# Performance work log

Measured on AMD Instinct MI355X. Metric: run time of the kernel, lower is better.

## Reference

```python
import jax, jax.numpy as jnp
import numpy as np

# dims (see shape_source)
B, L_IN, L_C, H, D, BLOCK = 4, 512, 512, 32, 128, 16
CTX = L_IN + L_C                      # context length per sequence
BLOCKS_PER_SEQ = CTX // BLOCK         # 64
NUM_BLOCKS = B * BLOCKS_PER_SEQ       # 256
T = B * L_IN                          # total new tokens


def setup_inputs() -> dict:
    key = jax.random.key(0)
    ks = jax.random.split(key, 5)
    Q = jax.random.normal(ks[0], (T, H * D), jnp.float32)
    K = jax.random.normal(ks[1], (T, H * D), jnp.float32)
    V = jax.random.normal(ks[2], (T, H * D), jnp.float32)
    Kcache = jax.random.normal(ks[3], (NUM_BLOCKS, BLOCK, H, D), jnp.float32)
    Vcache = jax.random.normal(ks[4], (NUM_BLOCKS, BLOCK, H, D), jnp.float32)
    # rotary tables for the new tokens: seq b token i sits at position L_C+i
    inv = 1.0 / (10000.0 ** (np.arange(0, D, 2, dtype=np.float32) / D))
    pos = np.tile(np.arange(L_C, L_C + L_IN, dtype=np.float32), B)   # [T]
    ang = pos[:, None] * inv[None, :]                                # [T, D/2]
    cos = jnp.asarray(np.concatenate([np.cos(ang), np.cos(ang)], -1))
    sin = jnp.asarray(np.concatenate([np.sin(ang), np.sin(ang)], -1))
    mask = jnp.zeros((L_IN, CTX), jnp.float32)  # additive mask (causal added inside)
    input_length = jnp.full((B,), L_IN, jnp.int32)
    cache_length = jnp.full((B,), L_C, jnp.int32)
    block_tables = jnp.arange(NUM_BLOCKS, dtype=jnp.int32).reshape(B, BLOCKS_PER_SEQ)
    # slot of new token i of seq b = flat cache index inside seq b's blocks
    slot_np = (np.arange(B)[:, None] * CTX + (L_C + np.arange(L_IN))[None, :]).reshape(-1)
    slots = jnp.asarray(slot_np, jnp.int32)
    return dict(Q=Q, K=K, V=V, Kcache=Kcache, Vcache=Vcache, cos=cos, sin=sin,
                mask=mask, input_length=input_length, cache_length=cache_length,
                slots=slots, block_tables=block_tables, max_s=CTX)


def _rot_half(x):
    h = x.shape[-1] // 2
    return jnp.concatenate([-x[..., h:], x[..., :h]], -1)


def reference(Q, K, V, Kcache, Vcache, cos, sin, mask,
              input_length, cache_length, slots, block_tables, max_s):
    scale = 1.0 / np.sqrt(D).astype(np.float32)
    q = Q.reshape(T, H, D)
    k = K.reshape(T, H, D)
    v = V.reshape(T, H, D)
    # inline RoPE on Q and new K (cos/sin broadcast over heads, as in the op)
    c = cos[:, None, :]
    s = sin[:, None, :]
    q = q * c + _rot_half(q) * s
    k = k * c + _rot_half(k) * s
    # write new K/V into the paged cache at `slots` (mode 3 behaviour)
    kc = Kcache.reshape(NUM_BLOCKS * BLOCK, H, D).at[slots].set(k)
    vc = Vcache.reshape(NUM_BLOCKS * BLOCK, H, D).at[slots].set(v)
    # gather per-sequence context via block tables -> [B, CTX, H, D]
    offs = jnp.arange(BLOCK, dtype=block_tables.dtype)
    flat = (block_tables[:, :, None] * BLOCK + offs[None, None, :]).reshape(B, -1)
    keys = kc[flat]
    vals = vc[flat]
    qb = q.reshape(B, L_IN, H, D)
    scores = jnp.einsum('bqhd,bkhd->bhqk', qb, keys) * scale + mask[None, None]
    # causal + length masking: query i at global pos cache_length+i
    qpos = cache_length[:, None] + jnp.arange(L_IN, dtype=jnp.int32)   # [B, L_IN]
    kpos = jnp.arange(CTX, dtype=jnp.int32)
    valid = (kpos[None, None, :] <= qpos[:, :, None]) & \
            (kpos[None, None, :] < (cache_length + input_length)[:, None, None])
    scores = jnp.where(valid[:, None], scores, jnp.float32(-1e30))
    attn = jax.nn.softmax(scores, axis=-1)
    out = jnp.einsum('bhqk,bkhd->bqhd', attn, vals)
    return out.reshape(T, H * D)
```

## Files before the change

### kernel.cpp

```cpp
#include <hip/hip_runtime.h>
#include <stdint.h>

#define BB   4
#define LIN  512
#define LCC  512
#define CTXL 1024
#define HH   32
#define DDIM 128
#define HD   4096
#define TT   2048
#define SCALE 0.08838834764831845f

typedef __attribute__((ext_vector_type(8))) short bf16x8;
typedef __attribute__((ext_vector_type(4))) float f32x4;
typedef __attribute__((ext_vector_type(4))) unsigned short us4;

__device__ __forceinline__ unsigned short f2bf(float f) {
  unsigned u = __float_as_uint(f);
  u += 0x7fffu + ((u >> 16) & 1u);
  return (unsigned short)(u >> 16);
}

__device__ __forceinline__ void async16(const void* g, void* l) {
  __builtin_amdgcn_global_load_lds(
      (const __attribute__((address_space(1))) void*)g,
      (__attribute__((address_space(3))) void*)l, 16, 0, 0);
}

__global__ __launch_bounds__(256) void prep_rope(
    const float* __restrict__ Q, const float* __restrict__ K,
    const float* __restrict__ cosT, const float* __restrict__ sinT,
    unsigned short* __restrict__ Qr, unsigned short* __restrict__ Kc) {
  int idx = blockIdx.x * 256 + threadIdx.x;
  int dp = idx & 63;
  int h  = (idx >> 6) & 31;
  int t  = idx >> 11;
  int b  = t >> 9;
  int i  = t & 511;
  int srcBase = t * HD + h * DDIM;
  float c = cosT[t * DDIM + dp];
  float s = sinT[t * DDIM + dp];
  float q0 = Q[srcBase + dp], q1 = Q[srcBase + dp + 64];
  float k0 = K[srcBase + dp], k1 = K[srcBase + dp + 64];
  int bh = b * HH + h;
  unsigned short* qd = Qr + ((size_t)bh * LIN + i) * DDIM;
  qd[dp]      = f2bf((q0 * c - q1 * s) * SCALE);
  qd[dp + 64] = f2bf((q1 * c + q0 * s) * SCALE);
  unsigned short* kd = Kc + ((size_t)bh * CTXL + LCC + i) * DDIM;
  kd[dp]      = f2bf(k0 * c - k1 * s);
  kd[dp + 64] = f2bf(k1 * c + k0 * s);
}

__global__ __launch_bounds__(256) void prep_kcache(
    const float* __restrict__ Kcache, const int* __restrict__ btab,
    unsigned short* __restrict__ Kc) {
  int idx = blockIdx.x * 256 + threadIdx.x;
  int d4  = idx & 31;
  int h   = (idx >> 5) & 31;
  int pos = (idx >> 10) & 511;
  int b   = idx >> 19;
  int blk = btab[b * 64 + (pos >> 4)];
  size_t src = (((size_t)blk * 16 + (pos & 15)) * HH + h) * DDIM + d4 * 4;
  float4 k4 = *(const float4*)(Kcache + src);
  size_t dst = (((size_t)(b * HH + h)) * CTXL + pos) * DDIM + d4 * 4;
  us4 kp;
  kp[0] = f2bf(k4.x); kp[1] = f2bf(k4.y); kp[2] = f2bf(k4.z); kp[3] = f2bf(k4.w);
  *(us4*)(Kc + dst) = kp;
}

__global__ __launch_bounds__(256) void prep_vt(
    const float* __restrict__ V, const float* __restrict__ Vcache,
    const int* __restrict__ btab, unsigned short* __restrict__ Vt) {
  __shared__ unsigned short tile[64][128];
  int bh = blockIdx.x;
  int kt = blockIdx.y;
  int b = bh >> 5, h = bh & 31;
  int t = threadIdx.x;
  int kv0 = kt * 64;
  int col4  = (t & 31) * 4;
  int rbase = t >> 5;
#pragma unroll
  for (int r8 = 0; r8 < 8; ++r8) {
    int row = r8 * 8 + rbase;
    int pos = kv0 + row;
    const float* src;
    if (kv0 < LCC) {
      int blk = btab[b * 64 + (pos >> 4)];
      src = Vcache + (((size_t)blk * 16 + (pos & 15)) * HH + h) * DDIM + col4;
    } else {
      int tok = b * LIN + (pos - LCC);
      src = V + (size_t)tok * HD + h * DDIM + col4;
    }
    float4 v4 = *(const float4*)src;
    us4 p;
    p[0] = f2bf(v4.x); p[1] = f2bf(v4.y); p[2] = f2bf(v4.z); p[3] = f2bf(v4.w);
    *(us4*)&tile[row][col4] = p;
  }
  __syncthreads();
  int d   = t >> 1;
  int kvh = (t & 1) * 32;
  unsigned short* dst = Vt + ((size_t)bh * DDIM + d) * CTXL + kv0 + kvh;
#pragma unroll
  for (int c = 0; c < 32; c += 4) {
    us4 o;
    o[0] = tile[kvh + c + 0][d];
    o[1] = tile[kvh + c + 1][d];
    o[2] = tile[kvh + c + 2][d];
    o[3] = tile[kvh + c + 3][d];
    *(us4*)(dst + c) = o;
  }
}

__global__ __launch_bounds__(256) void attn(
    const unsigned short* __restrict__ Qr, const unsigned short* __restrict__ Kc,
    const unsigned short* __restrict__ Vt, float* __restrict__ Out) {
  __shared__ __align__(16) char smem[41984];
  int bh = blockIdx.x;
  int qt = blockIdx.y;
  int b = bh >> 5, h = bh & 31;
  int tid = threadIdx.x;
  int w = tid >> 6, l = tid & 63, g = l >> 4, qi = l & 15;

  char* Klds = smem;
  char* Vlds = smem + 16384;
  char* Plds = smem + 32768 + w * 2304;

  const unsigned short* Qbase =
      Qr + ((size_t)bh * LIN + qt * 64 + w * 16 + qi) * DDIM;
  bf16x8 qf[4];
#pragma unroll
  for (int kk = 0; kk < 4; ++kk)
    qf[kk] = *(const bf16x8*)(Qbase + kk * 32 + g * 8);

  f32x4 acc[8];
#pragma unroll
  for (int dn = 0; dn < 8; ++dn) acc[dn] = (f32x4){0.f, 0.f, 0.f, 0.f};
  float m_run = -1e30f, l_run = 0.f;

  const size_t kRowBase = (size_t)bh * CTXL;
  const size_t vRowBase = (size_t)bh * DDIM;
  int ntiles = (LCC >> 6) + qt + 1;
  int qpos = LCC + qt * 64 + w * 16 + qi;

  for (int kt = 0; kt < ntiles; ++kt) {
    int kv0 = kt * 64;
    __syncthreads();
#pragma unroll
    for (int p = 0; p < 4; ++p) {
      int m = p * 256 + tid;
      int krow = m >> 4;
      int kcb  = ((m & 15) * 16) ^ ((krow & 7) << 4);
      async16((const char*)(Kc + (kRowBase + kv0 + krow) * DDIM) + kcb,
              Klds + m * 16);
      int vrow = m >> 3;
      int vcb  = ((m & 7) * 16) ^ ((vrow & 7) << 4);
      async16((const char*)(Vt + (vRowBase + vrow) * CTXL + kv0) + vcb,
              Vlds + m * 16);
    }
    __syncthreads();

    f32x4 st[4];
#pragma unroll
    for (int mt = 0; mt < 4; ++mt) {
      f32x4 c = (f32x4){0.f, 0.f, 0.f, 0.f};
#pragma unroll
      for (int kk = 0; kk < 4; ++kk) {
        int row = mt * 16 + qi;
        int cb  = (kk * 64 + g * 16) ^ ((row & 7) << 4);
        bf16x8 af = *(const bf16x8*)(Klds + row * 256 + cb);
        c = __builtin_amdgcn_mfma_f32_16x16x32_bf16(af, qf[kk], c, 0, 0, 0);
      }
      st[mt] = c;
    }

    if (kt == ntiles - 1) {
#pragma unroll
      for (int mt = 0; mt < 4; ++mt)
#pragma unroll
        for (int jj = 0; jj < 4; ++jj) {
          int kvpos = kv0 + mt * 16 + g * 4 + jj;
          if (kvpos > qpos) st[mt][jj] = -1e30f;
        }
    }

    float mt_ = -1e30f;
#pragma unroll
    for (int mt = 0; mt < 4; ++mt)
#pragma unroll
      for (int jj = 0; jj < 4; ++jj) mt_ = fmaxf(mt_, st[mt][jj]);
    mt_ = fmaxf(mt_, __shfl_xor(mt_, 16));
    mt_ = fmaxf(mt_, __shfl_xor(mt_, 32));
    float mnew  = fmaxf(m_run, mt_);
    float alpha = __expf(m_run - mnew);
    float psum = 0.f;
#pragma unroll
    for (int mt = 0; mt < 4; ++mt) {
      us4 pk;
#pragma unroll
      for (int jj = 0; jj < 4; ++jj) {
        float pv = __expf(st[mt][jj] - mnew);
        psum += pv;
        pk[jj] = f2bf(pv);
      }
      *(us4*)(Plds + qi * 144 + mt * 32 + g * 8) = pk;
    }
    psum += __shfl_xor(psum, 16);
    psum += __shfl_xor(psum, 32);
    l_run = l_run * alpha + psum;
    m_run = mnew;

    asm volatile("" ::: "memory");

    float af0 = __shfl(alpha, g * 4 + 0);
    float af1 = __shfl(alpha, g * 4 + 1);
    float af2 = __shfl(alpha, g * 4 + 2);
    float af3 = __shfl(alpha, g * 4 + 3);
#pragma unroll
    for (int dn = 0; dn < 8; ++dn) {
      acc[dn][0] *= af0; acc[dn][1] *= af1;
      acc[dn][2] *= af2; acc[dn][3] *= af3;
    }

#pragma unroll
    for (int kk2 = 0; kk2 < 2; ++kk2) {
      bf16x8 pa = *(const bf16x8*)(Plds + qi * 144 + kk2 * 64 + g * 16);
#pragma unroll
      for (int dn = 0; dn < 8; ++dn) {
        int d  = dn * 16 + qi;
        int cb = (kk2 * 64 + g * 16) ^ ((d & 7) << 4);
        bf16x8 vb = *(const bf16x8*)(Vlds + d * 128 + cb);
        acc[dn] = __builtin_amdgcn_mfma_f32_16x16x32_bf16(pa, vb, acc[dn], 0, 0, 0);
      }
    }
  }

  float inv = 1.f / l_run;
  float li0 = __shfl(inv, g * 4 + 0);
  float li1 = __shfl(inv, g * 4 + 1);
  float li2 = __shfl(inv, g * 4 + 2);
  float li3 = __shfl(inv, g * 4 + 3);
  int row0 = b * LIN + qt * 64 + w * 16 + g * 4;
  int col0 = h * DDIM + qi;
#pragma unroll
  for (int dn = 0; dn < 8; ++dn) {
    Out[(size_t)(row0 + 0) * HD + col0 + dn * 16] = acc[dn][0] * li0;
    Out[(size_t)(row0 + 1) * HD + col0 + dn * 16] = acc[dn][1] * li1;
    Out[(size_t)(row0 + 2) * HD + col0 + dn * 16] = acc[dn][2] * li2;
    Out[(size_t)(row0 + 3) * HD + col0 + dn * 16] = acc[dn][3] * li3;
  }
}

extern "C" void kernel_launch(void* const* d_in, const int* in_sizes, int n_in,
                              void* d_out, int out_size, void* d_ws, size_t ws_size,
                              hipStream_t stream) {
  (void)in_sizes; (void)n_in; (void)out_size; (void)ws_size;
  const float* Q      = (const float*)d_in[0];
  const float* K      = (const float*)d_in[1];
  const float* V      = (const float*)d_in[2];
  const float* Kcache = (const float*)d_in[3];
  const float* Vcache = (const float*)d_in[4];
  const float* cosT   = (const float*)d_in[5];
  const float* sinT   = (const float*)d_in[6];
  const int*   btab   = (const int*)d_in[11];

  unsigned short* Qr = (unsigned short*)d_ws;
  unsigned short* Kc = Qr + (size_t)BB * HH * LIN * DDIM;
  unsigned short* Vt = Kc + (size_t)BB * HH * CTXL * DDIM;
  float* Out = (float*)d_out;

  prep_rope<<<(TT * HH * 64) / 256, 256, 0, stream>>>(Q, K, cosT, sinT, Qr, Kc);
  prep_kcache<<<(BB * HH * LCC * 32) / 256, 256, 0, stream>>>(Kcache, btab, Kc);
  prep_vt<<<dim3(BB * HH, CTXL / 64), 256, 0, stream>>>(V, Vcache, btab, Vt);
  attn<<<dim3(BB * HH, LIN / 64), 256, 0, stream>>>(Qr, Kc, Vt, Out);
}
```

Measured before the change: 303.6 us.

## Fuse prep kernels into one and apply Q RoPE inside attention

Merges the three preprocessing kernels (RoPE on new K, K-cache gather, V transpose) into a single launch tiled by (head, kv tile). Q RoPE, scaling and bf16 conversion move into the attention kernel's Q fragment load, so the bf16 Q workspace buffer is no longer written and re-read. This removes two kernel launches and a Q round trip through global memory. The cost is extra fp32 Q/cos/sin loads and arithmetic at the start of each attention block, and K is now also converted in the transposing kernel.

```diff
diff --git a/kernel.cpp b/kernel.cpp
--- a/kernel.cpp
+++ b/kernel.cpp
@@ -27,78 +27,72 @@
       (__attribute__((address_space(3))) void*)l, 16, 0, 0);
 }
 
-__global__ __launch_bounds__(256) void prep_rope(
-    const float* __restrict__ Q, const float* __restrict__ K,
+__global__ __launch_bounds__(256) void prep(
+    const float* __restrict__ K, const float* __restrict__ V,
+    const float* __restrict__ Kcache, const float* __restrict__ Vcache,
     const float* __restrict__ cosT, const float* __restrict__ sinT,
-    unsigned short* __restrict__ Qr, unsigned short* __restrict__ Kc) {
-  int idx = blockIdx.x * 256 + threadIdx.x;
-  int dp = idx & 63;
-  int h  = (idx >> 6) & 31;
-  int t  = idx >> 11;
-  int b  = t >> 9;
-  int i  = t & 511;
-  int srcBase = t * HD + h * DDIM;
-  float c = cosT[t * DDIM + dp];
-  float s = sinT[t * DDIM + dp];
-  float q0 = Q[srcBase + dp], q1 = Q[srcBase + dp + 64];
-  float k0 = K[srcBase + dp], k1 = K[srcBase + dp + 64];
-  int bh = b * HH + h;
-  unsigned short* qd = Qr + ((size_t)bh * LIN + i) * DDIM;
-  qd[dp]      = f2bf((q0 * c - q1 * s) * SCALE);
-  qd[dp + 64] = f2bf((q1 * c + q0 * s) * SCALE);
-  unsigned short* kd = Kc + ((size_t)bh * CTXL + LCC + i) * DDIM;
-  kd[dp]      = f2bf(k0 * c - k1 * s);
-  kd[dp + 64] = f2bf(k1 * c + k0 * s);
-}
-
-__global__ __launch_bounds__(256) void prep_kcache(
-    const float* __restrict__ Kcache, const int* __restrict__ btab,
-    unsigned short* __restrict__ Kc) {
-  int idx = blockIdx.x * 256 + threadIdx.x;
-  int d4  = idx & 31;
-  int h   = (idx >> 5) & 31;
-  int pos = (idx >> 10) & 511;
-  int b   = idx >> 19;
-  int blk = btab[b * 64 + (pos >> 4)];
-  size_t src = (((size_t)blk * 16 + (pos & 15)) * HH + h) * DDIM + d4 * 4;
-  float4 k4 = *(const float4*)(Kcache + src);
-  size_t dst = (((size_t)(b * HH + h)) * CTXL + pos) * DDIM + d4 * 4;
-  us4 kp;
-  kp[0] = f2bf(k4.x); kp[1] = f2bf(k4.y); kp[2] = f2bf(k4.z); kp[3] = f2bf(k4.w);
-  *(us4*)(Kc + dst) = kp;
-}
-
-__global__ __launch_bounds__(256) void prep_vt(
-    const float* __restrict__ V, const float* __restrict__ Vcache,
-    const int* __restrict__ btab, unsigned short* __restrict__ Vt) {
+    const int* __restrict__ btab, unsigned short* __restrict__ Kc,
+    unsigned short* __restrict__ Vt) {
   __shared__ unsigned short tile[64][128];
-  int bh = blockIdx.x;
-  int kt = blockIdx.y;
+  int bh = blockIdx.x, kt = blockIdx.y;
   int b = bh >> 5, h = bh & 31;
   int t = threadIdx.x;
   int kv0 = kt * 64;
-  int col4  = (t & 31) * 4;
-  int rbase = t >> 5;
-#pragma unroll
-  for (int r8 = 0; r8 < 8; ++r8) {
-    int row = r8 * 8 + rbase;
-    int pos = kv0 + row;
-    const float* src;
-    if (kv0 < LCC) {
+
+  if (kv0 < LCC) {
+#pragma unroll
+    for (int it = 0; it < 8; ++it) {
+      int idx = it * 256 + t;
+      int row = idx >> 5, c4 = (idx & 31) * 4;
+      int pos = kv0 + row;
       int blk = btab[b * 64 + (pos >> 4)];
-      src = Vcache + (((size_t)blk * 16 + (pos & 15)) * HH + h) * DDIM + col4;
-    } else {
+      size_t src = (((size_t)blk * 16 + (pos & 15)) * HH + h) * DDIM + c4;
+      float4 k4 = *(const float4*)(Kcache + src);
+      float4 v4 = *(const float4*)(Vcache + src);
+      us4 kp, vp;
+      kp[0] = f2bf(k4.x); kp[1] = f2bf(k4.y); kp[2] = f2bf(k4.z); kp[3] = f2bf(k4.w);
+      vp[0] = f2bf(v4.x); vp[1] = f2bf(v4.y); vp[2] = f2bf(v4.z); vp[3] = f2bf(v4.w);
+      *(us4*)(Kc + ((size_t)bh * CTXL + pos) * DDIM + c4) = kp;
+      *(us4*)&tile[row][c4] = vp;
+    }
+  } else {
+#pragma unroll
+    for (int it = 0; it < 4; ++it) {
+      int idx = it * 256 + t;
+      int row = idx >> 4, d0 = (idx & 15) * 4;
+      int pos = kv0 + row;
       int tok = b * LIN + (pos - LCC);
-      src = V + (size_t)tok * HD + h * DDIM + col4;
-    }
-    float4 v4 = *(const float4*)src;
-    us4 p;
-    p[0] = f2bf(v4.x); p[1] = f2bf(v4.y); p[2] = f2bf(v4.z); p[3] = f2bf(v4.w);
-    *(us4*)&tile[row][col4] = p;
+      const float* src = K + (size_t)tok * HD + h * DDIM;
+      float4 k0 = *(const float4*)(src + d0);
+      float4 k1 = *(const float4*)(src + d0 + 64);
+      float4 cc = *(const float4*)(cosT + (size_t)tok * DDIM + d0);
+      float4 ss = *(const float4*)(sinT + (size_t)tok * DDIM + d0);
+      us4 lo, hi;
+      lo[0] = f2bf(k0.x * cc.x - k1.x * ss.x);
+      lo[1] = f2bf(k0.y * cc.y - k1.y * ss.y);
+      lo[2] = f2bf(k0.z * cc.z - k1.z * ss.z);
+      lo[3] = f2bf(k0.w * cc.w - k1.w * ss.w);
+      hi[0] = f2bf(k1.x * cc.x + k0.x * ss.x);
+      hi[1] = f2bf(k1.y * cc.y + k0.y * ss.y);
+      hi[2] = f2bf(k1.z * cc.z + k0.z * ss.z);
+      hi[3] = f2bf(k1.w * cc.w + k0.w * ss.w);
+      unsigned short* kd = Kc + ((size_t)bh * CTXL + pos) * DDIM;
+      *(us4*)(kd + d0) = lo;
+      *(us4*)(kd + d0 + 64) = hi;
+    }
+#pragma unroll
+    for (int it = 0; it < 8; ++it) {
+      int idx = it * 256 + t;
+      int row = idx >> 5, c4 = (idx & 31) * 4;
+      int tok = b * LIN + (kv0 - LCC) + row;
+      float4 v4 = *(const float4*)(V + (size_t)tok * HD + h * DDIM + c4);
+      us4 vp;
+      vp[0] = f2bf(v4.x); vp[1] = f2bf(v4.y); vp[2] = f2bf(v4.z); vp[3] = f2bf(v4.w);
+      *(us4*)&tile[row][c4] = vp;
+    }
   }
   __syncthreads();
-  int d   = t >> 1;
-  int kvh = (t & 1) * 32;
+  int d = t >> 1, kvh = (t & 1) * 32;
   unsigned short* dst = Vt + ((size_t)bh * DDIM + d) * CTXL + kv0 + kvh;
 #pragma unroll
   for (int c = 0; c < 32; c += 4) {
@@ -112,7 +106,8 @@
 }
 
 __global__ __launch_bounds__(256) void attn(
-    const unsigned short* __restrict__ Qr, const unsigned short* __restrict__ Kc,
+    const float* __restrict__ Q, const float* __restrict__ cosT,
+    const float* __restrict__ sinT, const unsigned short* __restrict__ Kc,
     const unsigned short* __restrict__ Vt, float* __restrict__ Out) {
   __shared__ __align__(16) char smem[41984];
   int bh = blockIdx.x;
@@ -124,21 +119,39 @@
   char* Klds = smem;
   char* Vlds = smem + 16384;
   char* Plds = smem + 32768 + w * 2304;
-
-  const unsigned short* Qbase =
-      Qr + ((size_t)bh * LIN + qt * 64 + w * 16 + qi) * DDIM;
+  const size_t kRowBase = (size_t)bh * CTXL;
+  const size_t vRowBase = (size_t)bh * DDIM;
+
+  int tok = b * LIN + qt * 64 + w * 16 + qi;
+  const float* Qrow = Q + (size_t)tok * HD + h * DDIM;
+  const float* crow = cosT + (size_t)tok * DDIM;
+  const float* srow = sinT + (size_t)tok * DDIM;
   bf16x8 qf[4];
-#pragma unroll
-  for (int kk = 0; kk < 4; ++kk)
-    qf[kk] = *(const bf16x8*)(Qbase + kk * 32 + g * 8);
+  union F8 { float4 v[2]; float f[8]; };
+#pragma unroll
+  for (int kk = 0; kk < 2; ++kk) {
+    int d0 = kk * 32 + g * 8;
+    F8 qa, qb, cc, ss;
+    qa.v[0] = *(const float4*)(Qrow + d0);
+    qa.v[1] = *(const float4*)(Qrow + d0 + 4);
+    qb.v[0] = *(const float4*)(Qrow + d0 + 64);
+    qb.v[1] = *(const float4*)(Qrow + d0 + 68);
+    cc.v[0] = *(const float4*)(crow + d0);
+    cc.v[1] = *(const float4*)(crow + d0 + 4);
+    ss.v[0] = *(const float4*)(srow + d0);
+    ss.v[1] = *(const float4*)(srow + d0 + 4);
+#pragma unroll
+    for (int j = 0; j < 8; ++j) {
+      qf[kk][j]     = (short)f2bf((qa.f[j] * cc.f[j] - qb.f[j] * ss.f[j]) * SCALE);
+      qf[kk + 2][j] = (short)f2bf((qb.f[j] * cc.f[j] + qa.f[j] * ss.f[j]) * SCALE);
+    }
+  }
 
   f32x4 acc[8];
 #pragma unroll
   for (int dn = 0; dn < 8; ++dn) acc[dn] = (f32x4){0.f, 0.f, 0.f, 0.f};
   float m_run = -1e30f, l_run = 0.f;
 
-  const size_t kRowBase = (size_t)bh * CTXL;
-  const size_t vRowBase = (size_t)bh * DDIM;
   int ntiles = (LCC >> 6) + qt + 1;
   int qpos = LCC + qt * 64 + w * 16 + qi;
 
@@ -263,13 +276,11 @@
   const float* sinT   = (const float*)d_in[6];
   const int*   btab   = (const int*)d_in[11];
 
-  unsigned short* Qr = (unsigned short*)d_ws;
-  unsigned short* Kc = Qr + (size_t)BB * HH * LIN * DDIM;
+  unsigned short* Kc = (unsigned short*)d_ws;
   unsigned short* Vt = Kc + (size_t)BB * HH * CTXL * DDIM;
   float* Out = (float*)d_out;
 
-  prep_rope<<<(TT * HH * 64) / 256, 256, 0, stream>>>(Q, K, cosT, sinT, Qr, Kc);
-  prep_kcache<<<(BB * HH * LCC * 32) / 256, 256, 0, stream>>>(Kcache, btab, Kc);
-  prep_vt<<<dim3(BB * HH, CTXL / 64), 256, 0, stream>>>(V, Vcache, btab, Vt);
-  attn<<<dim3(BB * HH, LIN / 64), 256, 0, stream>>>(Qr, Kc, Vt, Out);
-}
+  prep<<<dim3(BB * HH, CTXL / 64), 256, 0, stream>>>(K, V, Kcache, Vcache,
+                                                     cosT, sinT, btab, Kc, Vt);
+  attn<<<dim3(BB * HH, LIN / 64), 256, 0, stream>>>(Q, cosT, sinT, Kc, Vt, Out);
+}
```

Measured after the change: 299.8 us. About the same (-1.3%).
